# Kernel optimization log

Measured on AMD Instinct MI355X. Metric: run time of the kernel, lower is better.

The kernel has to match this reference:

```python
import jax, jax.numpy as jnp
import numpy as np

EMBED = 1024
HEADS = 16
HEAD_DIM = EMBED // HEADS


def setup_inputs() -> dict:
    key = jax.random.key(0)
    ks = jax.random.split(key, 12)
    B, S, E = 2, 2048, EMBED
    scale = 1.0 / np.sqrt(E)
    inp = {
        "query": jax.random.normal(ks[0], (B, S, E), jnp.float32),
        "key": jax.random.normal(ks[1], (B, S, E), jnp.float32),
        "value": jax.random.normal(ks[2], (B, S, E), jnp.float32),
        "Wq": jax.random.normal(ks[3], (E, E), jnp.float32) * scale,
        "bq": jax.random.normal(ks[4], (E,), jnp.float32) * 0.01,
        "Wk": jax.random.normal(ks[5], (E, E), jnp.float32) * scale,
        "bk": jax.random.normal(ks[6], (E,), jnp.float32) * 0.01,
        "Wv": jax.random.normal(ks[7], (E, E), jnp.float32) * scale,
        "bv": jax.random.normal(ks[8], (E,), jnp.float32) * 0.01,
        "Wo": jax.random.normal(ks[9], (E, E), jnp.float32) * scale,
        "bo": jax.random.normal(ks[10], (E,), jnp.float32) * 0.01,
    }
    return inp


def reference(query, key, value, Wq, bq, Wk, bk, Wv, bv, Wo, bo):
    B, Sq, E = query.shape
    Sk = key.shape[1]
    H, D = HEADS, HEAD_DIM
    # QKV projections (torch Linear: x @ W.T + b)
    q = (query @ Wq.T + bq).reshape(B, Sq, H, D)
    k = (key @ Wk.T + bk).reshape(B, Sk, H, D)
    v = (value @ Wv.T + bv).reshape(B, Sk, H, D)
    # energy: [B, H, Sq, Sk]; note scale = 1/sqrt(embed_size), not head_dim
    energy = jnp.einsum("bqhd,bkhd->bhqk", q, k)
    scale = jnp.asarray(E, energy.dtype) ** 0.5
    attn = jax.nn.softmax(energy / scale, axis=-1)
    out = jnp.einsum("bhqk,bkhd->bqhd", attn, v).reshape(B, Sq, E)
    # fc_out (dropout is identity at eval)
    return out @ Wo.T + bo
```

## Files before the change

kernel.cpp:

```cpp
#include <hip/hip_runtime.h>
#include <hip/hip_bf16.h>

typedef __hip_bfloat16 bf16;
typedef short frag8 __attribute__((ext_vector_type(8)));
typedef _Float16 half4 __attribute__((ext_vector_type(4)));
typedef _Float16 half8 __attribute__((ext_vector_type(8)));
typedef __fp16 fp16x2 __attribute__((ext_vector_type(2)));
typedef float f32x4 __attribute__((ext_vector_type(4)));

typedef __attribute__((address_space(3))) void lds_void;
typedef __attribute__((address_space(1))) const void gbl_void;

__device__ __forceinline__ void gld16(const void* g, void* l) {
  __builtin_amdgcn_global_load_lds((gbl_void*)g, (lds_void*)l, 16, 0, 0);
}

__device__ __forceinline__ unsigned short f2bf(float f) {
  union { float f; unsigned u; } x; x.f = f;
  unsigned r = x.u + 0x7FFFu + ((x.u >> 16) & 1u);
  return (unsigned short)(r >> 16);
}

#define QSCALE 0.0450842200278f
#define MFIX 4.0f

struct CvtArgs {
  const float4* src[7];
  ushort4* dst[7];
  int n4[7];
};
__global__ __launch_bounds__(256) void cvt_all(CvtArgs a) {
  const int t = blockIdx.y;
  const int i = blockIdx.x * 256 + threadIdx.x;
  if (i >= a.n4[t]) return;
  float4 v = a.src[t][i];
  ushort4 o;
  o.x = f2bf(v.x); o.y = f2bf(v.y); o.z = f2bf(v.z); o.w = f2bf(v.w);
  a.dst[t][i] = o;
}

template<int IH>
__device__ __forceinline__ void mfma16i(f32x4 (&acc)[8][4], const frag8 (&a4)[4], const frag8 (&b4)[4]) {
  __builtin_amdgcn_s_setprio(1);
  #pragma unroll
  for (int i = 0; i < 4; ++i) {
    #pragma unroll
    for (int j = 0; j < 4; ++j)
      acc[IH * 4 + i][j] = __builtin_amdgcn_mfma_f32_16x16x32_bf16(a4[i], b4[j], acc[IH * 4 + i][j], 0, 0, 0);
  }
  __builtin_amdgcn_s_setprio(0);
}

__global__ __launch_bounds__(512, 2)
void gemm_qkv256(const bf16* __restrict__ A0, const bf16* __restrict__ A1, const bf16* __restrict__ A2,
                 const bf16* __restrict__ W0, const bf16* __restrict__ W1, const bf16* __restrict__ W2,
                 const float* __restrict__ b0, const float* __restrict__ b1, const float* __restrict__ b2,
                 void* __restrict__ o0, void* __restrict__ o1, void* __restrict__ o2) {
  __shared__ __align__(16) bf16 As[2][16384];
  __shared__ __align__(16) bf16 Bs[2][16384];
  const int tid = threadIdx.x;
  const int wave = tid >> 6, lane = tid & 63, quad = lane >> 4, l16 = lane & 15;
  const int wm = wave >> 2, wn = wave & 3;
  const int bn = blockIdx.x, bm = blockIdx.y, z = blockIdx.z;

  const bf16* A = A0; const bf16* W = W0; const float* bias = b0; void* out = o0;
  if (z == 1) { A = A1; W = W1; bias = b1; out = o1; }
  else if (z == 2) { A = A2; W = W2; bias = b2; out = o2; }

  const bf16* Ab = A + (size_t)bm * 256 * 1024;
  const bf16* Wb = W + (size_t)bn * 256 * 1024;
  const int c0_ = tid & 3, r0_ = tid >> 2;
  const int gcp = ((c0_ ^ ((r0_ >> 1) & 3)) << 3);
  const int rc2 = (quad ^ ((l16 >> 1) & 3)) << 3;

  auto stage = [&](const bf16* src, int kt, int kh, bf16* dst) {
    #pragma unroll
    for (int is = 0; is < 2; ++is) {
      const int r = r0_ + is * 128;
      gld16(src + (size_t)r * 1024 + kt * 64 + kh * 32 + gcp,
            (void*)(dst + (is * 512 + tid) * 8));
    }
  };
  auto ldsA4 = [&](const bf16* ah, int ih, frag8 (&a4)[4]) {
    #pragma unroll
    for (int i = 0; i < 4; ++i)
      a4[i] = *(const frag8*)&ah[(wm * 128 + ih * 64 + i * 16 + l16) * 32 + rc2];
  };
  auto ldsB4 = [&](const bf16* bh, frag8 (&b4)[4]) {
    #pragma unroll
    for (int j = 0; j < 4; ++j)
      b4[j] = *(const frag8*)&bh[(wn * 64 + j * 16 + l16) * 32 + rc2];
  };

  f32x4 acc[8][4];
  #pragma unroll
  for (int i = 0; i < 8; ++i)
    #pragma unroll
    for (int j = 0; j < 4; ++j)
      acc[i][j] = (f32x4){0.f, 0.f, 0.f, 0.f};

  stage(Ab, 0, 0, &As[0][0]);
  stage(Wb, 0, 0, &Bs[0][0]);
  stage(Ab, 0, 1, &As[0][8192]);
  stage(Wb, 0, 1, &Bs[0][8192]);
  asm volatile("s_waitcnt vmcnt(0)" ::: "memory");
  __builtin_amdgcn_s_barrier();

  #pragma unroll 2
  for (int t = 0; t < 15; ++t) {
    const int buf = t & 1, nb = buf ^ 1;
    const bf16* a0 = &As[buf][0];    const bf16* a1 = &As[buf][8192];
    const bf16* b0 = &Bs[buf][0];    const bf16* b1 = &Bs[buf][8192];
    frag8 af[4], bf4[4];

    ldsA4(a0, 0, af); ldsB4(b0, bf4);
    stage(Ab, t + 1, 0, &As[nb][0]);
    __builtin_amdgcn_s_barrier();
    asm volatile("s_waitcnt lgkmcnt(0)" ::: "memory");
    mfma16i<0>(acc, af, bf4);
    __builtin_amdgcn_s_barrier();

    ldsA4(a0, 1, af);
    stage(Wb, t + 1, 0, &Bs[nb][0]);
    asm volatile("s_waitcnt vmcnt(4)" ::: "memory");
    __builtin_amdgcn_s_barrier();
    asm volatile("s_waitcnt lgkmcnt(0)" ::: "memory");
    mfma16i<1>(acc, af, bf4);
    __builtin_amdgcn_s_barrier();

    ldsA4(a1, 0, af); ldsB4(b1, bf4);
    stage(Ab, t + 1, 1, &As[nb][8192]);
    __builtin_amdgcn_s_barrier();
    asm volatile("s_waitcnt lgkmcnt(0)" ::: "memory");
    mfma16i<0>(acc, af, bf4);
    __builtin_amdgcn_s_barrier();

    ldsA4(a1, 1, af);
    stage(Wb, t + 1, 1, &Bs[nb][8192]);
    asm volatile("s_waitcnt vmcnt(4)" ::: "memory");
    __builtin_amdgcn_s_barrier();
    asm volatile("s_waitcnt lgkmcnt(0)" ::: "memory");
    mfma16i<1>(acc, af, bf4);
    __builtin_amdgcn_s_barrier();
  }

  {
    const bf16* a0 = &As[1][0];    const bf16* a1 = &As[1][8192];
    const bf16* b0 = &Bs[1][0];    const bf16* b1 = &Bs[1][8192];
    frag8 af[4], bf4[4];
    ldsA4(a0, 0, af); ldsB4(b0, bf4);
    asm volatile("s_waitcnt lgkmcnt(0)" ::: "memory");
    mfma16i<0>(acc, af, bf4);
    ldsA4(a0, 1, af);
    asm volatile("s_waitcnt lgkmcnt(0)" ::: "memory");
    mfma16i<1>(acc, af, bf4);
    asm volatile("s_waitcnt vmcnt(0)" ::: "memory");
    __builtin_amdgcn_s_barrier();
    ldsA4(a1, 0, af); ldsB4(b1, bf4);
    asm volatile("s_waitcnt lgkmcnt(0)" ::: "memory");
    mfma16i<0>(acc, af, bf4);
    ldsA4(a1, 1, af);
    asm volatile("s_waitcnt lgkmcnt(0)" ::: "memory");
    mfma16i<1>(acc, af, bf4);
  }

  #pragma unroll
  for (int j = 0; j < 4; ++j) {
    const int col = bn * 256 + wn * 64 + j * 16 + l16;
    const float bv = bias[col];
    #pragma unroll
    for (int i = 0; i < 8; ++i) {
      #pragma unroll
      for (int r = 0; r < 4; ++r) {
        const int row = bm * 256 + wm * 128 + i * 16 + quad * 4 + r;
        float v = acc[i][j][r] + bv;
        const int b = row >> 11, s = row & 2047;
        const int hh = col >> 6, d = col & 63;
        const size_t bh = (size_t)(b * 16 + hh);
        if (z == 0) {
          v *= QSCALE;
          ((bf16*)out)[(bh * 2048 + s) * 64 + d] = __float2bfloat16(v);
        } else if (z == 1) {
          const int g = s >> 6, l32 = s & 31, G32 = (s >> 5) & 1;
          const int q_ = (l32 >> 3) & 3, t_ = (l32 >> 2) & 1, i_ = l32 & 3;
          const int r64 = G32 * 32 + t_ * 16 + q_ * 4 + i_;
          const size_t addr = bh * 131072 + (size_t)g * 4096 + (size_t)r64 * 64
                            + (size_t)(((d >> 3) ^ (r64 & 7)) << 3) + (d & 7);
          ((bf16*)out)[addr] = __float2bfloat16(v);
        } else {
          const int g = s >> 6, k = s & 63;
          const size_t addr = bh * 131072 + (size_t)g * 4096 + (size_t)d * 64
                            + (size_t)(((k >> 3) ^ (d & 7)) << 3) + (k & 7);
          ((_Float16*)out)[addr] = (_Float16)v;
        }
      }
    }
  }
}

template<int MODE>
__global__ __launch_bounds__(256)
void gemm_bt(const bf16* __restrict__ A0, const bf16* __restrict__ A1, const bf16* __restrict__ A2,
             const bf16* __restrict__ W0, const bf16* __restrict__ W1, const bf16* __restrict__ W2,
             const float* __restrict__ b0, const float* __restrict__ b1, const float* __restrict__ b2,
             void* __restrict__ o0, void* __restrict__ o1, void* __restrict__ o2) {
  constexpr int NK = 1024;
  constexpr int BN = (MODE == 1) ? 128 : 64;
  __shared__ __align__(16) bf16 As[2][128 * 32];
  __shared__ __align__(16) bf16 Bs[2][BN * 32];
  const int tid = threadIdx.x;
  const int wave = tid >> 6, lane = tid & 63, quad = lane >> 4, l16 = lane & 15;
  const int wm = wave >> 1, wn = wave & 1;
  const int bn = blockIdx.x, bm = blockIdx.y;

  const bf16* A = A0; const bf16* W = W0; const float* bias = b0; void* out = o0;

  const bf16* Ab = A + (size_t)bm * 128 * NK;
  const bf16* Wb = W + (size_t)bn * BN * NK;
  const int c0_ = tid & 3, r0_ = tid >> 2;
  const int rc = (quad ^ (l16 & 3)) << 3;

  auto stageA = [&](int k0, int buf) {
    #pragma unroll
    for (int is = 0; is < 2; ++is) {
      const int c = tid + is * 256;
      const int r = r0_ + is * 64;
      const int gc = (c0_ ^ (r & 3)) << 3;
      gld16(Ab + (size_t)r * NK + k0 + gc, (void*)(&As[buf][(size_t)c * 8]));
    }
  };
  auto stageW = [&](int k0, int buf) {
    const int r = r0_;
    const int gc = (c0_ ^ (r & 3)) << 3;
    gld16(Wb + (size_t)r * NK + k0 + gc, (void*)(&Bs[buf][(size_t)tid * 8]));
  };

  f32x4 acc[4][2];
  #pragma unroll
  for (int i = 0; i < 4; ++i)
    #pragma unroll
    for (int j = 0; j < 2; ++j)
      acc[i][j] = (f32x4){0.f, 0.f, 0.f, 0.f};

  stageA(0, 0); stageW(0, 0);
  #pragma unroll 2
  for (int kt = 0; kt < 32; ++kt) {
    __syncthreads();
    if (kt < 31) { stageA((kt + 1) * 32, (kt + 1) & 1); stageW((kt + 1) * 32, (kt + 1) & 1); }
    const bf16* as_ = As[kt & 1];
    const bf16* bs_ = Bs[kt & 1];
    frag8 af[4], bfr[2];
    #pragma unroll
    for (int i = 0; i < 4; ++i)
      af[i] = *(const frag8*)&as_[(wm * 64 + i * 16 + l16) * 32 + rc];
    #pragma unroll
    for (int j = 0; j < 2; ++j)
      bfr[j] = *(const frag8*)&bs_[(wn * 32 + j * 16 + l16) * 32 + rc];
    #pragma unroll
    for (int i = 0; i < 4; ++i)
      #pragma unroll
      for (int j = 0; j < 2; ++j)
        acc[i][j] = __builtin_amdgcn_mfma_f32_16x16x32_bf16(af[i], bfr[j], acc[i][j], 0, 0, 0);
  }

  #pragma unroll
  for (int j = 0; j < 2; ++j) {
    const int col = bn * 64 + wn * 32 + j * 16 + l16;
    const float bv = bias[col];
    #pragma unroll
    for (int i = 0; i < 4; ++i) {
      #pragma unroll
      for (int r = 0; r < 4; ++r) {
        const int row = bm * 128 + wm * 64 + i * 16 + quad * 4 + r;
        ((float*)out)[(size_t)row * 1024 + col] = acc[i][j][r] + bv;
      }
    }
  }
}

__global__ __launch_bounds__(512, 2)
void flash_attn(const bf16* __restrict__ Q, const bf16* __restrict__ K,
                const _Float16* __restrict__ Vt, bf16* __restrict__ ctx) {
  __shared__ __align__(16) char smem[65536];
  bf16* Ks = (bf16*)smem;
  _Float16* Vs = (_Float16*)(smem + 32768);
  const int tid = threadIdx.x;
  const int wave = tid >> 6, lane = tid & 63, quad = lane >> 4, l16 = lane & 15;
  const int qg = wave & 3, kvg = wave >> 2;
  const int bh = blockIdx.x, b = bh >> 4, h = bh & 15;
  const int q0 = blockIdx.y * 256 + qg * 64;
  const bf16* Qb = Q + (size_t)bh * 131072;
  const bf16* Kb = K + (size_t)bh * 131072;
  const _Float16* Vb = Vt + (size_t)bh * 131072;

  frag8 qf[4][2];
  #pragma unroll
  for (int qt = 0; qt < 4; ++qt)
    #pragma unroll
    for (int ks = 0; ks < 2; ++ks)
      qf[qt][ks] = *(const frag8*)(Qb + (size_t)(q0 + qt * 16 + l16) * 64 + ks * 32 + quad * 8);

  f32x4 rsv[4];
  f32x4 o[4][4];
  #pragma unroll
  for (int qt = 0; qt < 4; ++qt) {
    rsv[qt] = (f32x4){0.f, 0.f, 0.f, 0.f};
    #pragma unroll
    for (int dt = 0; dt < 4; ++dt)
      o[qt][dt] = (f32x4){0.f, 0.f, 0.f, 0.f};
  }

  const int xk = l16 & 7;

  auto stage = [&](int kt, int buf) {
    #pragma unroll
    for (int s = 0; s < 2; ++s) {
      const int g = s * 16 + kt;
      gld16(Kb + (size_t)g * 4096 + (size_t)tid * 8, (void*)(Ks + (s * 2 + buf) * 4096 + tid * 8));
      gld16(Vb + (size_t)g * 4096 + (size_t)tid * 8, (void*)(Vs + (s * 2 + buf) * 4096 + tid * 8));
    }
  };

  stage(0, 0);
  #pragma unroll 2
  for (int kt = 0; kt < 16; ++kt) {
    __syncthreads();
    if (kt < 15) stage(kt + 1, (kt + 1) & 1);
    const bf16* ks_ = Ks + (kvg * 2 + (kt & 1)) * 4096;
    const _Float16* vs_ = Vs + (kvg * 2 + (kt & 1)) * 4096;

    f32x4 s[4][4];
    #pragma unroll
    for (int qt = 0; qt < 4; ++qt)
      #pragma unroll
      for (int jt = 0; jt < 4; ++jt)
        s[qt][jt] = (f32x4){-MFIX, -MFIX, -MFIX, -MFIX};
    #pragma unroll
    for (int ks = 0; ks < 2; ++ks) {
      frag8 kf[4];
      #pragma unroll
      for (int jt = 0; jt < 4; ++jt)
        kf[jt] = *(const frag8*)&ks_[(jt * 16 + l16) * 64 + (((ks * 4 + quad) ^ xk) << 3)];
      __builtin_amdgcn_s_setprio(1);
      #pragma unroll
      for (int qt = 0; qt < 4; ++qt)
        #pragma unroll
        for (int jt = 0; jt < 4; ++jt)
          s[qt][jt] = __builtin_amdgcn_mfma_f32_16x16x32_bf16(kf[jt], qf[qt][ks], s[qt][jt], 0, 0, 0);
      __builtin_amdgcn_s_setprio(0);
    }

    half8 pb[4][2];
    #pragma unroll
    for (int qt = 0; qt < 4; ++qt) {
      #pragma unroll
      for (int jt = 0; jt < 4; ++jt) {
        f32x4 p4;
        #pragma unroll
        for (int r = 0; r < 4; ++r)
          p4[r] = __builtin_amdgcn_exp2f(s[qt][jt][r]);
        rsv[qt] += p4;
        union { fp16x2 h2[2]; half4 h4; } u;
        u.h2[0] = __builtin_amdgcn_cvt_pkrtz(p4[0], p4[1]);
        u.h2[1] = __builtin_amdgcn_cvt_pkrtz(p4[2], p4[3]);
        const int jtp = jt >> 1, hi = (jt & 1) * 4;
        pb[qt][jtp][hi + 0] = u.h4[0];
        pb[qt][jtp][hi + 1] = u.h4[1];
        pb[qt][jtp][hi + 2] = u.h4[2];
        pb[qt][jtp][hi + 3] = u.h4[3];
      }
    }

    #pragma unroll
    for (int jtp = 0; jtp < 2; ++jtp) {
      half8 vf[4];
      #pragma unroll
      for (int dt = 0; dt < 4; ++dt)
        vf[dt] = *(const half8*)&vs_[(dt * 16 + l16) * 64 + (((jtp * 4 + quad) ^ xk) << 3)];
      __builtin_amdgcn_s_setprio(1);
      #pragma unroll
      for (int qt = 0; qt < 4; ++qt)
        #pragma unroll
        for (int dt = 0; dt < 4; ++dt)
          o[qt][dt] = __builtin_amdgcn_mfma_f32_16x16x32_f16(vf[dt], pb[qt][jtp], o[qt][dt], 0, 0, 0);
      __builtin_amdgcn_s_setprio(0);
    }
  }

  float4* mo = (float4*)smem;
  float*  ml = (float*)(smem + 32768);
  const int mbase = (qg * 64 + lane) * 8;
  #pragma unroll
  for (int r = 0; r < 2; ++r) {
    __syncthreads();
    if (kvg == 1) {
      #pragma unroll
      for (int qh = 0; qh < 2; ++qh) {
        const int qt = r * 2 + qh;
        #pragma unroll
        for (int dt = 0; dt < 4; ++dt) {
          const int i = qh * 4 + dt;
          mo[mbase + (i ^ (lane & 7))] = (float4){o[qt][dt][0], o[qt][dt][1], o[qt][dt][2], o[qt][dt][3]};
        }
        ml[(qg * 64 + lane) * 2 + qh] = rsv[qt][0] + rsv[qt][1] + rsv[qt][2] + rsv[qt][3];
      }
    }
    __syncthreads();
    if (kvg == 0) {
      #pragma unroll
      for (int qh = 0; qh < 2; ++qh) {
        const int qt = r * 2 + qh;
        float l = rsv[qt][0] + rsv[qt][1] + rsv[qt][2] + rsv[qt][3]
                + ml[(qg * 64 + lane) * 2 + qh];
        l += __shfl_xor(l, 16, 64);
        l += __shfl_xor(l, 32, 64);
        const float inv = __builtin_amdgcn_rcpf(l);
        const int q = q0 + qt * 16 + l16;
        #pragma unroll
        for (int dt = 0; dt < 4; ++dt) {
          const int i = qh * 4 + dt;
          const float4 po = mo[mbase + (i ^ (lane & 7))];
          ushort4 w;
          w.x = f2bf((o[qt][dt][0] + po.x) * inv);
          w.y = f2bf((o[qt][dt][1] + po.y) * inv);
          w.z = f2bf((o[qt][dt][2] + po.z) * inv);
          w.w = f2bf((o[qt][dt][3] + po.w) * inv);
          const int d = dt * 16 + quad * 4;
          *(uint2*)&ctx[((size_t)(b * 2048 + q)) * 1024 + h * 64 + d] = *(uint2*)&w;
        }
      }
    }
  }
}

extern "C" void kernel_launch(void* const* d_in, const int* in_sizes, int n_in,
                              void* d_out, int out_size, void* d_ws, size_t ws_size,
                              hipStream_t stream) {
  const float* q_in = (const float*)d_in[0];
  const float* k_in = (const float*)d_in[1];
  const float* v_in = (const float*)d_in[2];
  const float* Wq = (const float*)d_in[3];
  const float* bq = (const float*)d_in[4];
  const float* Wk = (const float*)d_in[5];
  const float* bk = (const float*)d_in[6];
  const float* Wv = (const float*)d_in[7];
  const float* bv = (const float*)d_in[8];
  const float* Wo = (const float*)d_in[9];
  const float* bo = (const float*)d_in[10];

  char* ws = (char*)d_ws;
  const size_t MB = 1024 * 1024;
  bf16* Xq  = (bf16*)(ws + 0 * MB);
  bf16* Xk  = (bf16*)(ws + 8 * MB);
  bf16* Xv  = (bf16*)(ws + 16 * MB);
  bf16* Wqb = (bf16*)(ws + 24 * MB);
  bf16* Wkb = (bf16*)(ws + 26 * MB);
  bf16* Wvb = (bf16*)(ws + 28 * MB);
  bf16* Wob = (bf16*)(ws + 30 * MB);
  bf16* Qw  = (bf16*)(ws + 32 * MB);
  bf16* Kw  = (bf16*)(ws + 40 * MB);
  _Float16* Vtw = (_Float16*)(ws + 48 * MB);
  bf16* Ctx = (bf16*)(ws + 56 * MB);

  {
    CvtArgs a;
    a.src[0] = (const float4*)q_in; a.dst[0] = (ushort4*)Xq;  a.n4[0] = 4194304 / 4;
    a.src[1] = (const float4*)k_in; a.dst[1] = (ushort4*)Xk;  a.n4[1] = 4194304 / 4;
    a.src[2] = (const float4*)v_in; a.dst[2] = (ushort4*)Xv;  a.n4[2] = 4194304 / 4;
    a.src[3] = (const float4*)Wq;   a.dst[3] = (ushort4*)Wqb; a.n4[3] = 1048576 / 4;
    a.src[4] = (const float4*)Wk;   a.dst[4] = (ushort4*)Wkb; a.n4[4] = 1048576 / 4;
    a.src[5] = (const float4*)Wv;   a.dst[5] = (ushort4*)Wvb; a.n4[5] = 1048576 / 4;
    a.src[6] = (const float4*)Wo;   a.dst[6] = (ushort4*)Wob; a.n4[6] = 1048576 / 4;
    cvt_all<<<dim3(4096, 7), 256, 0, stream>>>(a);
  }

  gemm_qkv256<<<dim3(4, 16, 3), 512, 0, stream>>>(Xq, Xk, Xv, Wqb, Wkb, Wvb,
                                                  bq, bk, bv, Qw, Kw, (bf16*)Vtw);
  flash_attn<<<dim3(32, 8), 512, 0, stream>>>(Qw, Kw, Vtw, Ctx);
  gemm_bt<0><<<dim3(16, 32), 256, 0, stream>>>(Ctx, nullptr, nullptr, Wob, nullptr, nullptr,
                                               bo, nullptr, nullptr, d_out, nullptr, nullptr);
}
```

Baseline: 227.3 us.

## Simplify QKV GEMM main loop to one barrier per k-tile with bulk prefetch

Replaces the fine-grained four-phase schedule, which interleaved LDS loads, global prefetches and many barriers, with a simpler loop. It issues all next-tile global-to-LDS loads up front, then loads 8 A fragments and 4 B fragments per half and runs 32 MFMAs per half, with a single vmcnt(0) wait and barrier per iteration. The aim is to cut barrier and waitcnt overhead. The trade-offs are higher register pressure from 8 live A fragments, less fine-grained overlap of LDS reads with MFMAs, and dropping the loop unroll from 2 to 1.

```diff
diff --git a/kernel.cpp b/kernel.cpp
--- a/kernel.cpp
+++ b/kernel.cpp
@@ -39,14 +39,13 @@
   a.dst[t][i] = o;
 }
 
-template<int IH>
-__device__ __forceinline__ void mfma16i(f32x4 (&acc)[8][4], const frag8 (&a4)[4], const frag8 (&b4)[4]) {
+__device__ __forceinline__ void mfma32(f32x4 (&acc)[8][4], const frag8 (&a8)[8], const frag8 (&b4)[4]) {
   __builtin_amdgcn_s_setprio(1);
   #pragma unroll
-  for (int i = 0; i < 4; ++i) {
+  for (int i = 0; i < 8; ++i) {
     #pragma unroll
     for (int j = 0; j < 4; ++j)
-      acc[IH * 4 + i][j] = __builtin_amdgcn_mfma_f32_16x16x32_bf16(a4[i], b4[j], acc[IH * 4 + i][j], 0, 0, 0);
+      acc[i][j] = __builtin_amdgcn_mfma_f32_16x16x32_bf16(a8[i], b4[j], acc[i][j], 0, 0, 0);
   }
   __builtin_amdgcn_s_setprio(0);
 }
@@ -81,10 +80,10 @@
             (void*)(dst + (is * 512 + tid) * 8));
     }
   };
-  auto ldsA4 = [&](const bf16* ah, int ih, frag8 (&a4)[4]) {
-    #pragma unroll
-    for (int i = 0; i < 4; ++i)
-      a4[i] = *(const frag8*)&ah[(wm * 128 + ih * 64 + i * 16 + l16) * 32 + rc2];
+  auto ldsA8 = [&](const bf16* ah, frag8 (&a8)[8]) {
+    #pragma unroll
+    for (int i = 0; i < 8; ++i)
+      a8[i] = *(const frag8*)&ah[(wm * 128 + i * 16 + l16) * 32 + rc2];
   };
   auto ldsB4 = [&](const bf16* bh, frag8 (&b4)[4]) {
     #pragma unroll
@@ -106,62 +105,35 @@
   asm volatile("s_waitcnt vmcnt(0)" ::: "memory");
   __builtin_amdgcn_s_barrier();
 
-  #pragma unroll 2
+  #pragma unroll 1
   for (int t = 0; t < 15; ++t) {
     const int buf = t & 1, nb = buf ^ 1;
     const bf16* a0 = &As[buf][0];    const bf16* a1 = &As[buf][8192];
     const bf16* b0 = &Bs[buf][0];    const bf16* b1 = &Bs[buf][8192];
-    frag8 af[4], bf4[4];
-
-    ldsA4(a0, 0, af); ldsB4(b0, bf4);
+
     stage(Ab, t + 1, 0, &As[nb][0]);
-    __builtin_amdgcn_s_barrier();
-    asm volatile("s_waitcnt lgkmcnt(0)" ::: "memory");
-    mfma16i<0>(acc, af, bf4);
-    __builtin_amdgcn_s_barrier();
-
-    ldsA4(a0, 1, af);
     stage(Wb, t + 1, 0, &Bs[nb][0]);
-    asm volatile("s_waitcnt vmcnt(4)" ::: "memory");
-    __builtin_amdgcn_s_barrier();
-    asm volatile("s_waitcnt lgkmcnt(0)" ::: "memory");
-    mfma16i<1>(acc, af, bf4);
-    __builtin_amdgcn_s_barrier();
-
-    ldsA4(a1, 0, af); ldsB4(b1, bf4);
     stage(Ab, t + 1, 1, &As[nb][8192]);
-    __builtin_amdgcn_s_barrier();
-    asm volatile("s_waitcnt lgkmcnt(0)" ::: "memory");
-    mfma16i<0>(acc, af, bf4);
-    __builtin_amdgcn_s_barrier();
-
-    ldsA4(a1, 1, af);
     stage(Wb, t + 1, 1, &Bs[nb][8192]);
-    asm volatile("s_waitcnt vmcnt(4)" ::: "memory");
-    __builtin_amdgcn_s_barrier();
-    asm volatile("s_waitcnt lgkmcnt(0)" ::: "memory");
-    mfma16i<1>(acc, af, bf4);
+
+    frag8 a8[8], b4[4];
+    ldsA8(a0, a8); ldsB4(b0, b4);
+    mfma32(acc, a8, b4);
+    ldsA8(a1, a8); ldsB4(b1, b4);
+    mfma32(acc, a8, b4);
+
+    asm volatile("s_waitcnt vmcnt(0)" ::: "memory");
     __builtin_amdgcn_s_barrier();
   }
 
   {
     const bf16* a0 = &As[1][0];    const bf16* a1 = &As[1][8192];
     const bf16* b0 = &Bs[1][0];    const bf16* b1 = &Bs[1][8192];
-    frag8 af[4], bf4[4];
-    ldsA4(a0, 0, af); ldsB4(b0, bf4);
-    asm volatile("s_waitcnt lgkmcnt(0)" ::: "memory");
-    mfma16i<0>(acc, af, bf4);
-    ldsA4(a0, 1, af);
-    asm volatile("s_waitcnt lgkmcnt(0)" ::: "memory");
-    mfma16i<1>(acc, af, bf4);
-    asm volatile("s_waitcnt vmcnt(0)" ::: "memory");
-    __builtin_amdgcn_s_barrier();
-    ldsA4(a1, 0, af); ldsB4(b1, bf4);
-    asm volatile("s_waitcnt lgkmcnt(0)" ::: "memory");
-    mfma16i<0>(acc, af, bf4);
-    ldsA4(a1, 1, af);
-    asm volatile("s_waitcnt lgkmcnt(0)" ::: "memory");
-    mfma16i<1>(acc, af, bf4);
+    frag8 a8[8], b4[4];
+    ldsA8(a0, a8); ldsB4(b0, b4);
+    mfma32(acc, a8, b4);
+    ldsA8(a1, a8); ldsB4(b1, b4);
+    mfma32(acc, a8, b4);
   }
 
   #pragma unroll
```

New measurement: 236.7 us. 4.2% more time.
